# Kernel tuning notes

Hardware: AMD Instinct MI355X
Metric: run time of the kernel (lower is better)

## Reference

```python
import jax, jax.numpy as jnp
import numpy as np


def setup_inputs() -> dict:
    key = jax.random.key(0)
    kx, kw, kb = jax.random.split(key, 3)
    B, D, L, W = 2, 4096, 4096, 4
    # int8 quantized input / weight / bias (stored as int8, full [-128,127] range)
    x = jax.random.randint(kx, (B, D, L), -128, 128, dtype=jnp.int32).astype(jnp.int8)
    weight = jax.random.randint(kw, (D, W), -128, 128, dtype=jnp.int32).astype(jnp.int8)
    bias = jax.random.randint(kb, (D,), -128, 128, dtype=jnp.int32).astype(jnp.int8)
    return {
        "x": x,
        "weight": weight,
        "bias": bias,
        "input_scale": jnp.float32(0.05),
        "weight_scale": jnp.float32(0.002),
        "output_scale": jnp.float32(0.05),
        "bias_scale": jnp.float32(0.01),
    }


def _causal_dw_conv(xf, wf):
    # xf: [B, D, L] float, wf: [D, W] float; depthwise causal conv (left pad W-1)
    D, W = wf.shape
    return jax.lax.conv_general_dilated(
        xf, wf[:, None, :],  # [D, 1, W] OIH with feature_group_count=D -> depthwise
        window_strides=(1,), padding=[(W - 1, 0)],
        dimension_numbers=("NCH", "OIH", "NCH"), feature_group_count=D)


def reference(x, weight, bias, input_scale, weight_scale, output_scale, bias_scale):
    # fused dequant -> causal depthwise conv -> bias -> SiLU -> requant to int8
    xf = x.astype(jnp.float32) * input_scale
    wf = weight.astype(jnp.float32) * weight_scale
    bf = bias.astype(jnp.float32) * bias_scale
    y = _causal_dw_conv(xf, wf) + bf[None, :, None]
    y = jax.nn.silu(y)  # causal_conv1d activation=True -> SiLU
    q = jnp.clip(jnp.round(y / output_scale), -128.0, 127.0).astype(jnp.int8)
    return q
```

## Files before the change

### kernel.cpp

```cpp
#include <hip/hip_runtime.h>


#define DMASK 4095

typedef int iv4 __attribute__((ext_vector_type(4)));

__device__ __forceinline__ int silu_requant(float y, float inv_out) {
    float e = __expf(-y);
    float s = y * __builtin_amdgcn_rcpf(1.0f + e);
    float q = rintf(s * inv_out);
    q = fminf(fmaxf(q, -128.0f), 127.0f);
    return (int)q;
}

__global__ __launch_bounds__(256) void qconv1d_kernel(
    const int* __restrict__ x,
    const int* __restrict__ w,
    const int* __restrict__ bias,
    const float* __restrict__ in_s_p,
    const float* __restrict__ w_s_p,
    const float* __restrict__ out_s_p,
    const float* __restrict__ b_s_p,
    int* __restrict__ out)
{
    const int tid  = threadIdx.x;
    const int row  = blockIdx.x;
    const int d    = row & DMASK;
    const int rcb  = row << 10;

    const iv4* __restrict__ xv = (const iv4*)x;

    iv4 cur[4], prv[4];
#pragma unroll
    for (int j = 0; j < 4; ++j)
        cur[j] = xv[rcb + (j << 8) + tid];

    {
        iv4 p = (iv4){0, 0, 0, 0};
        if (tid != 0) p = xv[rcb + tid - 1];
        prv[0] = p;
    }
#pragma unroll
    for (int j = 1; j < 4; ++j)
        prv[j] = xv[rcb + (j << 8) + tid - 1];

    iv4 wv = ((const iv4*)w)[d];
    const float w0 = (float)wv.x, w1 = (float)wv.y, w2 = (float)wv.z, w3 = (float)wv.w;
    const float bias_i = (float)bias[d];

    const float in_s  = in_s_p[0];
    const float w_s   = w_s_p[0];
    const float out_s = out_s_p[0];
    const float b_s   = b_s_p[0];

    const float s_xw    = in_s * w_s;
    const float inv_out = 1.0f / out_s;
    const float bf      = bias_i * b_s;

    iv4* __restrict__ ov = (iv4*)out;

#pragma unroll
    for (int j = 0; j < 4; ++j) {
        float sm3 = (float)prv[j].y, sm2 = (float)prv[j].z, sm1 = (float)prv[j].w;
        float s0 = (float)cur[j].x, s1 = (float)cur[j].y,
              s2 = (float)cur[j].z, s3 = (float)cur[j].w;

        float a0 = w0*sm3 + w1*sm2 + w2*sm1 + w3*s0;
        float a1 = w0*sm2 + w1*sm1 + w2*s0  + w3*s1;
        float a2 = w0*sm1 + w1*s0  + w2*s1  + w3*s2;
        float a3 = w0*s0  + w1*s1  + w2*s2  + w3*s3;

        iv4 q;
        q.x = silu_requant(a0 * s_xw + bf, inv_out);
        q.y = silu_requant(a1 * s_xw + bf, inv_out);
        q.z = silu_requant(a2 * s_xw + bf, inv_out);
        q.w = silu_requant(a3 * s_xw + bf, inv_out);

        ov[rcb + (j << 8) + tid] = q;
    }
}

extern "C" void kernel_launch(void* const* d_in, const int* in_sizes, int n_in,
                              void* d_out, int out_size, void* d_ws, size_t ws_size,
                              hipStream_t stream) {
    const int*   x    = (const int*)d_in[0];
    const int*   w    = (const int*)d_in[1];
    const int*   bias = (const int*)d_in[2];
    const float* is   = (const float*)d_in[3];
    const float* ws   = (const float*)d_in[4];
    const float* os   = (const float*)d_in[5];
    const float* bs   = (const float*)d_in[6];
    int* out = (int*)d_out;

    const int rows  = out_size >> 12;
    const int block = 256;

    qconv1d_kernel<<<rows, block, 0, stream>>>(x, w, bias, is, ws, os, bs, out);
}
```

Measured before the change: 236.9 us.

## Share conv halo through LDS, split rows across two blocks, nontemporal stores

Each thread previously reloaded the preceding 16-byte vector from global memory to get the causal halo. Now the block stages its contiguous input chunk in shared memory and reads the previous vector from there, which removes the duplicate global loads. Each row is split across two blocks, doubling the grid for more parallelism, and outputs use nontemporal stores. The cost is one barrier and an LDS round-trip per block.

```diff
diff --git a/kernel.cpp b/kernel.cpp
--- a/kernel.cpp
+++ b/kernel.cpp
@@ -23,60 +23,62 @@
     const float* __restrict__ b_s_p,
     int* __restrict__ out)
 {
+    __shared__ iv4 ldsv[513];
+
     const int tid  = threadIdx.x;
-    const int row  = blockIdx.x;
+    const int bid  = blockIdx.x;
+    const int row  = bid >> 1;
+    const int half = bid & 1;
     const int d    = row & DMASK;
-    const int rcb  = row << 10;
+    const int gcb  = (row << 10) + (half << 9);
 
     const iv4* __restrict__ xv = (const iv4*)x;
 
-    iv4 cur[4], prv[4];
-#pragma unroll
-    for (int j = 0; j < 4; ++j)
-        cur[j] = xv[rcb + (j << 8) + tid];
-
-    {
-        iv4 p = (iv4){0, 0, 0, 0};
-        if (tid != 0) p = xv[rcb + tid - 1];
-        prv[0] = p;
+    iv4 a0 = xv[gcb + tid];
+    iv4 a1 = xv[gcb + 256 + tid];
+    if (tid == 0) {
+        iv4 hh = (iv4){0, 0, 0, 0};
+        if (half) hh = xv[gcb - 1];
+        ldsv[0] = hh;
     }
-#pragma unroll
-    for (int j = 1; j < 4; ++j)
-        prv[j] = xv[rcb + (j << 8) + tid - 1];
+    ldsv[1 + tid]       = a0;
+    ldsv[1 + 256 + tid] = a1;
 
     iv4 wv = ((const iv4*)w)[d];
     const float w0 = (float)wv.x, w1 = (float)wv.y, w2 = (float)wv.z, w3 = (float)wv.w;
     const float bias_i = (float)bias[d];
+    const float s_xw    = in_s_p[0] * w_s_p[0];
+    const float inv_out = 1.0f / out_s_p[0];
+    const float bf      = bias_i * b_s_p[0];
 
-    const float in_s  = in_s_p[0];
-    const float w_s   = w_s_p[0];
-    const float out_s = out_s_p[0];
-    const float b_s   = b_s_p[0];
+    __syncthreads();
 
-    const float s_xw    = in_s * w_s;
-    const float inv_out = 1.0f / out_s;
-    const float bf      = bias_i * b_s;
+    iv4 h0 = ldsv[tid];
+    iv4 h1 = ldsv[256 + tid];
 
     iv4* __restrict__ ov = (iv4*)out;
 
 #pragma unroll
-    for (int j = 0; j < 4; ++j) {
-        float sm3 = (float)prv[j].y, sm2 = (float)prv[j].z, sm1 = (float)prv[j].w;
-        float s0 = (float)cur[j].x, s1 = (float)cur[j].y,
-              s2 = (float)cur[j].z, s3 = (float)cur[j].w;
+    for (int j = 0; j < 2; ++j) {
+        iv4 cur = j ? a1 : a0;
+        iv4 h   = j ? h1 : h0;
 
-        float a0 = w0*sm3 + w1*sm2 + w2*sm1 + w3*s0;
-        float a1 = w0*sm2 + w1*sm1 + w2*s0  + w3*s1;
-        float a2 = w0*sm1 + w1*s0  + w2*s1  + w3*s2;
-        float a3 = w0*s0  + w1*s1  + w2*s2  + w3*s3;
+        float sm3 = (float)h.y, sm2 = (float)h.z, sm1 = (float)h.w;
+        float s0 = (float)cur.x, s1 = (float)cur.y,
+              s2 = (float)cur.z, s3 = (float)cur.w;
+
+        float a_0 = w0*sm3 + w1*sm2 + w2*sm1 + w3*s0;
+        float a_1 = w0*sm2 + w1*sm1 + w2*s0  + w3*s1;
+        float a_2 = w0*sm1 + w1*s0  + w2*s1  + w3*s2;
+        float a_3 = w0*s0  + w1*s1  + w2*s2  + w3*s3;
 
         iv4 q;
-        q.x = silu_requant(a0 * s_xw + bf, inv_out);
-        q.y = silu_requant(a1 * s_xw + bf, inv_out);
-        q.z = silu_requant(a2 * s_xw + bf, inv_out);
-        q.w = silu_requant(a3 * s_xw + bf, inv_out);
+        q.x = silu_requant(a_0 * s_xw + bf, inv_out);
+        q.y = silu_requant(a_1 * s_xw + bf, inv_out);
+        q.z = silu_requant(a_2 * s_xw + bf, inv_out);
+        q.w = silu_requant(a_3 * s_xw + bf, inv_out);
 
-        ov[rcb + (j << 8) + tid] = q;
+        __builtin_nontemporal_store(q, &ov[gcb + (j << 8) + tid]);
     }
 }
 
@@ -93,7 +95,8 @@
     int* out = (int*)d_out;
 
     const int rows  = out_size >> 12;
+    const int grid  = rows << 1;
     const int block = 256;
 
-    qconv1d_kernel<<<rows, block, 0, stream>>>(x, w, bias, is, ws, os, bs, out);
+    qconv1d_kernel<<<grid, block, 0, stream>>>(x, w, bias, is, ws, os, bs, out);
 }
```

After: 240.5 us. About the same (+1.5%).
